# Kernel optimization log

Measured on AMD Instinct MI355X. Metric: run time of the kernel, lower is better.

The kernel has to match this reference:

```python
import jax, jax.numpy as jnp
import numpy as np

B, C, H, W, K = 2, 64, 192, 384, 8

def setup_inputs():
    key = jax.random.key(0)
    k1, k2, k3, k4, k5, k6 = jax.random.split(key, 6)
    feat = jax.random.normal(k1, (B, C, H, W), dtype=jnp.float32)
    mask_high = jax.random.randint(k2, (B, 1, H, W), 0, 2).astype(bool)
    Wo = jax.random.normal(k3, (2 * K, C), dtype=jnp.float32) * 0.1  # offset_conv 1x1 weight
    bo = jax.random.normal(k4, (2 * K,), dtype=jnp.float32) * 0.1
    Ww = jax.random.normal(k5, (K, C), dtype=jnp.float32) * 0.1     # weight_conv 1x1 weight
    bw = jax.random.normal(k6, (K,), dtype=jnp.float32) * 0.1
    return {"feat": feat, "mask_high": mask_high, "Wo": Wo, "bo": bo, "Ww": Ww, "bw": bw}

def _bilinear_sample(feat, px, py):
    # feat [B,C,H,W]; px,py [B,K,H,W] in pixel coords.
    # Matches F.grid_sample(mode='bilinear', padding_mode='zeros', align_corners=True)
    Bs, Cs, Hs, Ws = feat.shape
    Ks = px.shape[1]
    x0 = jnp.floor(px); y0 = jnp.floor(py)
    wx = px - x0; wy = py - y0
    x0i = x0.astype(jnp.int32); y0i = y0.astype(jnp.int32)
    feat_flat = feat.reshape(Bs, 1, Cs, Hs * Ws)
    def corner(xi, yi, w):
        valid = (xi >= 0) & (xi < Ws) & (yi >= 0) & (yi < Hs)
        idx = jnp.clip(yi, 0, Hs - 1) * Ws + jnp.clip(xi, 0, Ws - 1)
        g = jnp.take_along_axis(feat_flat, idx.reshape(Bs, Ks, 1, Hs * Ws), axis=-1)
        g = g.reshape(Bs, Ks, Cs, Hs, Ws)
        return g * (w * valid)[:, :, None]  # zero out-of-bounds corners
    return (corner(x0i, y0i, (1 - wx) * (1 - wy))
            + corner(x0i + 1, y0i, wx * (1 - wy))
            + corner(x0i, y0i + 1, (1 - wx) * wy)
            + corner(x0i + 1, y0i + 1, wx * wy))

def reference(feat, mask_high, Wo, bo, Ww, bw):
    Bs, Cs, Hs, Ws = feat.shape
    # 1x1 convs as channel contractions
    offsets = jnp.einsum('oc,bchw->bohw', Wo, feat) + bo[None, :, None, None]  # [B,2K,H,W]
    logits = jnp.einsum('kc,bchw->bkhw', Ww, feat) + bw[None, :, None, None]   # [B,K,H,W]
    weights = jax.nn.softmax(logits, axis=1)
    # base grid linspace(-1,1) with align_corners=True maps exactly to pixel coords;
    # dx/((W-1)/2) in normalized space == dx pixels, so sample point = (x+dx, y+dy)
    xs = jnp.arange(Ws, dtype=feat.dtype)
    ys = jnp.arange(Hs, dtype=feat.dtype)
    px = xs[None, None, None, :] + offsets[:, 0::2]  # [B,K,H,W]
    py = ys[None, None, :, None] + offsets[:, 1::2]
    sampled = _bilinear_sample(feat, px, py)          # [B,K,C,H,W]
    residual = jnp.einsum('bkchw,bkhw->bchw', sampled, weights)
    return feat + residual * mask_high.astype(feat.dtype)
```

## Files before the change

kernel.cpp:

```cpp
#include <hip/hip_runtime.h>
#include <hip/hip_fp16.h>

#define B_ 2
#define C_ 64
#define H_ 192
#define W_ 384
#define K_ 8
constexpr int HW_ = H_ * W_;
constexpr int CHW_ = C_ * HW_;
constexpr int NP_ = B_ * HW_;
constexpr int NBLK_ = NP_ / 64;
constexpr size_t WS_NEED_ = (size_t)NP_ * 64 * sizeof(unsigned short);

typedef _Float16 h8 __attribute__((ext_vector_type(8)));
typedef float f32x4 __attribute__((ext_vector_type(4)));

static __device__ __forceinline__ __half2 u2h(uint u) {
  union { uint u; __half2 h; } x; x.u = u; return x.h;
}
static __device__ __forceinline__ uint h2u(__half2 h) {
  union { uint u; __half2 h; } x; x.h = h; return x.u;
}

__global__ __launch_bounds__(256) void transposeh_kernel(
    const float* __restrict__ feat, unsigned short* __restrict__ ft) {
  __shared__ float lds[64 * 65];
  const int tid = threadIdx.x;
  const int lane = tid & 63;
  const int wv = tid >> 6;
  const int bid = blockIdx.x;
  const int sb = (bid & 7) * (NBLK_ / 8) + (bid >> 3);
  const int p0 = sb * 64;
  const int b = p0 / HW_;
  const int hw0 = p0 - b * HW_;
  const float* fb = feat + (size_t)b * CHW_;
#pragma unroll
  for (int cc = 0; cc < 16; ++cc) {
    const int c = wv * 16 + cc;
    lds[lane * 65 + c] = fb[(size_t)c * HW_ + hw0 + lane];
  }
  __syncthreads();
  uint* ft32 = (uint*)ft;
#pragma unroll
  for (int j = 0; j < 8; ++j) {
    const int idx = j * 256 + tid;
    const int row = idx >> 5;
    const int cp = idx & 31;
    const __half2 h = __floats2half2_rn(lds[row * 65 + 2 * cp],
                                        lds[row * 65 + 2 * cp + 1]);
    ft32[(size_t)(p0 + row) * 32 + cp] = h2u(h);
  }
}

__global__ __launch_bounds__(256) void mega_kernel(
    const int* __restrict__ mask,
    const float* __restrict__ Wo, const float* __restrict__ bo,
    const float* __restrict__ Ww, const float* __restrict__ bw,
    const unsigned short* __restrict__ ws, float* __restrict__ out) {
  __shared__ uint smem[6272];
  const unsigned short* sth = (const unsigned short*)smem;
  float* clds = (float*)(smem + 2304);
  uint4* reco = (uint4*)smem;
  uint4* recw = (uint4*)(smem + 2048);
  uint* resb = smem + 4096;
  int* actl = (int*)(smem + 6208);

  const int tid = threadIdx.x;
  const int lane = tid & 63;
  const int wv = tid >> 6;
  const int bid = blockIdx.x;
  const int sb = (bid & 7) * (NBLK_ / 8) + (bid >> 3);
  const int p0 = sb * 64;
  const int b = p0 / HW_;
  const int hw0 = p0 - b * HW_;
  const size_t bCHW = (size_t)b * CHW_;
  const int bHW = b * HW_;

  const uint4* ftq = (const uint4*)ws;
#pragma unroll
  for (int e = 0; e < 2; ++e) {
    const int j = tid * 2 + e;
    const int row = j >> 3;
    const int q = j & 7;
    const uint4 v = ftq[(size_t)p0 * 8 + j];
    *(uint4*)(smem + row * 36 + q * 4) = v;
  }
  const bool act = (mask[p0 + lane] != 0);
  const unsigned long long mball = __ballot(act);
  const int A = __popcll(mball);
#pragma unroll
  for (int j = 0; j < 9; ++j) {
    const int idx = j * 256 + tid;
    if (idx < 2112) resb[idx] = 0u;
  }
  __syncthreads();

  const int mrow = lane & 15;
  const int kq = lane >> 4;
  h8 afr[2][2];
#pragma unroll
  for (int mt = 0; mt < 2; ++mt) {
    const int row = mt * 16 + mrow;
    const float* wrow = (row < 16) ? (Wo + row * 64)
                                   : (Ww + (((row - 16) < 8 ? (row - 16) : 7) * 64));
    const float z = (row < 24) ? 1.f : 0.f;
#pragma unroll
    for (int k0 = 0; k0 < 2; ++k0) {
      const float4 a = *(const float4*)(wrow + k0 * 32 + kq * 8);
      const float4 bq = *(const float4*)(wrow + k0 * 32 + kq * 8 + 4);
      h8 h;
      h[0] = (_Float16)(a.x * z);  h[1] = (_Float16)(a.y * z);
      h[2] = (_Float16)(a.z * z);  h[3] = (_Float16)(a.w * z);
      h[4] = (_Float16)(bq.x * z); h[5] = (_Float16)(bq.y * z);
      h[6] = (_Float16)(bq.z * z); h[7] = (_Float16)(bq.w * z);
      afr[mt][k0] = h;
    }
  }
  const int px = wv * 16 + mrow;
  f32x4 ac0 = {0.f, 0.f, 0.f, 0.f};
  f32x4 ac1 = {0.f, 0.f, 0.f, 0.f};
#pragma unroll
  for (int k0 = 0; k0 < 2; ++k0) {
    const h8 bf = *(const h8*)(sth + px * 72 + k0 * 32 + kq * 8);
    ac0 = __builtin_amdgcn_mfma_f32_16x16x32_f16(afr[0][k0], bf, ac0, 0, 0, 0);
    ac1 = __builtin_amdgcn_mfma_f32_16x16x32_f16(afr[1][k0], bf, ac1, 0, 0, 0);
  }
#pragma unroll
  for (int r = 0; r < 4; ++r) clds[(kq * 4 + r) * 64 + px] = ac0[r];
  if (kq < 2) {
#pragma unroll
    for (int r = 0; r < 4; ++r) clds[(16 + kq * 4 + r) * 64 + px] = ac1[r];
  }
  __syncthreads();

  float acc[24];
#pragma unroll
  for (int j = 0; j < 24; ++j) acc[j] = clds[j * 64 + lane];
  __syncthreads();

#pragma unroll
  for (int j = 0; j < 16; ++j) acc[j] += bo[j];
#pragma unroll
  for (int j = 0; j < 8; ++j) acc[16 + j] += bw[j];
  float m = acc[16];
#pragma unroll
  for (int k = 1; k < K_; ++k) m = fmaxf(m, acc[16 + k]);
  float s = 0.f;
#pragma unroll
  for (int k = 0; k < K_; ++k) s += __expf(acc[16 + k] - m);
  const float inv = (act ? 1.f : 0.f) / s;

  const int hw = hw0 + lane;
  const int y = hw / W_;
  const int x = hw - y * W_;

#pragma unroll
  for (int t = 0; t < 2; ++t) {
    const int k = wv * 2 + t;
    const float wtk = __expf(acc[16 + k] - m) * inv;
    const float pxf = (float)x + acc[2 * k];
    const float pyf = (float)y + acc[2 * k + 1];
    const float x0f = floorf(pxf), y0f = floorf(pyf);
    const float wx = pxf - x0f, wy = pyf - y0f;
    const int x0 = (int)x0f, y0 = (int)y0f;
    const int x1 = x0 + 1, y1 = y0 + 1;
    const bool vx0 = ((unsigned)x0 < (unsigned)W_);
    const bool vx1 = ((unsigned)x1 < (unsigned)W_);
    const bool vy0 = ((unsigned)y0 < (unsigned)H_);
    const bool vy1 = ((unsigned)y1 < (unsigned)H_);
    const int cx0 = min(max(x0, 0), W_ - 1), cx1 = min(max(x1, 0), W_ - 1);
    const int cy0 = min(max(y0, 0), H_ - 1), cy1 = min(max(y1, 0), H_ - 1);
    const float w00 = wtk * (1.f - wx) * (1.f - wy) * ((vx0 && vy0) ? 1.f : 0.f);
    const float w01 = wtk * wx * (1.f - wy) * ((vx1 && vy0) ? 1.f : 0.f);
    const float w10 = wtk * (1.f - wx) * wy * ((vx0 && vy1) ? 1.f : 0.f);
    const float w11 = wtk * wx * wy * ((vx1 && vy1) ? 1.f : 0.f);
    uint4 o;
    o.x = act ? (uint)((bHW + cy0 * W_ + cx0) << 7) : 0u;
    o.y = act ? (uint)((bHW + cy0 * W_ + cx1) << 7) : 0u;
    o.z = act ? (uint)((bHW + cy1 * W_ + cx0) << 7) : 0u;
    o.w = act ? (uint)((bHW + cy1 * W_ + cx1) << 7) : 0u;
    uint4 wq;
    wq.x = h2u(__float2half2_rn(w00));
    wq.y = h2u(__float2half2_rn(w01));
    wq.z = h2u(__float2half2_rn(w10));
    wq.w = h2u(__float2half2_rn(w11));
    reco[k * 64 + lane] = o;
    recw[k * 64 + lane] = wq;
  }
  {
    const int aidx = __builtin_amdgcn_mbcnt_hi(
        (unsigned)(mball >> 32), __builtin_amdgcn_mbcnt_lo((unsigned)mball, 0));
    if (act) actl[aidx] = lane;
    if (A > 0) {
      const int first = __ffsll((unsigned long long)mball) - 1;
      if (lane >= A) actl[lane] = first;
    }
  }
  __syncthreads();

  const int pg = lane >> 3;
  const int cg = lane & 7;
  const int cgb = cg * 16;
  const char* ftb = (const char*)ws;
  const int tot = (A + 7) >> 3;

#define ACCH(V, WU)                                                        \
  do {                                                                     \
    const __half2 wh_ = u2h(WU);                                           \
    rr0 = __hfma2(wh_, u2h((V).x), rr0);                                   \
    rr1 = __hfma2(wh_, u2h((V).y), rr1);                                   \
    rr2 = __hfma2(wh_, u2h((V).z), rr2);                                   \
    rr3 = __hfma2(wh_, u2h((V).w), rr3);                                   \
  } while (0)

  for (int i = wv; i < tot; i += 4) {
    const int gi = i * 8 + pg;
    const int pxl = actl[gi];
    __half2 rr0 = __float2half2_rn(0.f), rr1 = rr0, rr2 = rr0, rr3 = rr0;
#pragma unroll
    for (int k2 = 0; k2 < 4; ++k2) {
      const int k0 = 2 * k2, k1 = 2 * k2 + 1;
      const uint4 o0 = reco[k0 * 64 + pxl];
      const uint4 w0 = recw[k0 * 64 + pxl];
      const uint4 o1 = reco[k1 * 64 + pxl];
      const uint4 w1 = recw[k1 * 64 + pxl];
      const uint4 v0 = *(const uint4*)(ftb + (o0.x + cgb));
      const uint4 v1 = *(const uint4*)(ftb + (o0.y + cgb));
      const uint4 v2 = *(const uint4*)(ftb + (o0.z + cgb));
      const uint4 v3 = *(const uint4*)(ftb + (o0.w + cgb));
      const uint4 v4 = *(const uint4*)(ftb + (o1.x + cgb));
      const uint4 v5 = *(const uint4*)(ftb + (o1.y + cgb));
      const uint4 v6 = *(const uint4*)(ftb + (o1.z + cgb));
      const uint4 v7 = *(const uint4*)(ftb + (o1.w + cgb));
      ACCH(v0, w0.x); ACCH(v1, w0.y); ACCH(v2, w0.z); ACCH(v3, w0.w);
      ACCH(v4, w1.x); ACCH(v5, w1.y); ACCH(v6, w1.z); ACCH(v7, w1.w);
    }
    if (gi < A) {
      const int base = pxl * 33 + cg * 4;
      resb[base + 0] = h2u(rr0);
      resb[base + 1] = h2u(rr1);
      resb[base + 2] = h2u(rr2);
      resb[base + 3] = h2u(rr3);
    }
  }
#undef ACCH
  __syncthreads();

  const uint* ft32 = (const uint*)ws;
  const size_t ftrow = (size_t)(p0 + lane) * 32;
#pragma unroll
  for (int cc = 0; cc < 8; ++cc) {
    const int cp = wv * 8 + cc;
    const float2 fv = __half22float2(u2h(ft32[ftrow + cp]));
    const float2 rv = __half22float2(u2h(resb[lane * 33 + cp]));
    const size_t off = bCHW + (size_t)(2 * cp) * HW_ + hw0 + lane;
    out[off] = fv.x + rv.x;
    out[off + HW_] = fv.y + rv.y;
  }
}

__global__ __launch_bounds__(256) void fused_kernel(
    const float* __restrict__ feat, const int* __restrict__ mask,
    const float* __restrict__ Wo, const float* __restrict__ bo,
    const float* __restrict__ Ww, const float* __restrict__ bw,
    float* __restrict__ out) {
  const int p = blockIdx.x * blockDim.x + threadIdx.x;
  const int b = p / HW_;
  const int hw = p - b * HW_;
  const int y = hw / W_;
  const int x = hw - y * W_;
  const float* fb = feat + b * CHW_;
  float acc[24];
#pragma unroll
  for (int i = 0; i < 16; ++i) acc[i] = bo[i];
#pragma unroll
  for (int i = 0; i < 8; ++i) acc[16 + i] = bw[i];
#pragma unroll
  for (int c = 0; c < C_; ++c) {
    const float v = fb[c * HW_ + hw];
#pragma unroll
    for (int i = 0; i < 16; ++i) acc[i] = fmaf(Wo[i * C_ + c], v, acc[i]);
#pragma unroll
    for (int i = 0; i < 8; ++i) acc[16 + i] = fmaf(Ww[i * C_ + c], v, acc[16 + i]);
  }
  float m = acc[16];
#pragma unroll
  for (int k = 1; k < K_; ++k) m = fmaxf(m, acc[16 + k]);
  float wt[K_];
  float s = 0.f;
#pragma unroll
  for (int k = 0; k < K_; ++k) { wt[k] = __expf(acc[16 + k] - m); s += wt[k]; }
  const float fm = (mask[p] != 0) ? 1.f : 0.f;
  const float inv = fm / s;
#pragma unroll
  for (int k = 0; k < K_; ++k) wt[k] *= inv;
  float res[C_];
#pragma unroll
  for (int c = 0; c < C_; ++c) res[c] = 0.f;
  if (fm != 0.f) {
#pragma unroll
    for (int k = 0; k < K_; ++k) {
      const float px = (float)x + acc[2 * k];
      const float py = (float)y + acc[2 * k + 1];
      const float x0f = floorf(px), y0f = floorf(py);
      const float wx = px - x0f, wy = py - y0f;
      const int x0 = (int)x0f, y0 = (int)y0f;
      const int x1 = x0 + 1, y1 = y0 + 1;
      const bool vx0 = ((unsigned)x0 < (unsigned)W_);
      const bool vx1 = ((unsigned)x1 < (unsigned)W_);
      const bool vy0 = ((unsigned)y0 < (unsigned)H_);
      const bool vy1 = ((unsigned)y1 < (unsigned)H_);
      const int cx0 = min(max(x0, 0), W_ - 1), cx1 = min(max(x1, 0), W_ - 1);
      const int cy0 = min(max(y0, 0), H_ - 1), cy1 = min(max(y1, 0), H_ - 1);
      const float wk = wt[k];
      const float w00 = wk * (1.f - wx) * (1.f - wy) * ((vx0 && vy0) ? 1.f : 0.f);
      const float w01 = wk * wx * (1.f - wy) * ((vx1 && vy0) ? 1.f : 0.f);
      const float w10 = wk * (1.f - wx) * wy * ((vx0 && vy1) ? 1.f : 0.f);
      const float w11 = wk * wx * wy * ((vx1 && vy1) ? 1.f : 0.f);
      const int i00 = cy0 * W_ + cx0, i01 = cy0 * W_ + cx1;
      const int i10 = cy1 * W_ + cx0, i11 = cy1 * W_ + cx1;
#pragma unroll
      for (int c = 0; c < C_; ++c) {
        const float* fc = fb + c * HW_;
        res[c] += w00 * fc[i00] + w01 * fc[i01] + w10 * fc[i10] + w11 * fc[i11];
      }
    }
  }
#pragma unroll
  for (int c = 0; c < C_; ++c)
    out[b * CHW_ + c * HW_ + hw] = fb[c * HW_ + hw] + res[c];
}

extern "C" void kernel_launch(void* const* d_in, const int* in_sizes, int n_in,
                              void* d_out, int out_size, void* d_ws, size_t ws_size,
                              hipStream_t stream) {
  const float* feat = (const float*)d_in[0];
  const int* mask = (const int*)d_in[1];
  const float* Wo = (const float*)d_in[2];
  const float* bo = (const float*)d_in[3];
  const float* Ww = (const float*)d_in[4];
  const float* bw = (const float*)d_in[5];
  float* out = (float*)d_out;

  if (ws_size >= WS_NEED_) {
    unsigned short* ft = (unsigned short*)d_ws;
    hipLaunchKernelGGL(transposeh_kernel, dim3(NBLK_), dim3(256), 0, stream,
                       feat, ft);
    hipLaunchKernelGGL(mega_kernel, dim3(NBLK_), dim3(256), 0, stream,
                       mask, Wo, bo, Ww, bw, ft, out);
  } else {
    hipLaunchKernelGGL(fused_kernel, dim3(NP_ / 256), dim3(256), 0, stream,
                       feat, mask, Wo, bo, Ww, bw, out);
  }
}
```

Before: 42.17 us.

## Read MFMA operands from global, pack bilinear weights, trim LDS and a barrier

Drops the LDS staging of the 64-pixel fp16 feature tile and loads the MFMA B fragments directly from global memory, which removes one __syncthreads and shrinks shared memory. The active-pixel list is built earlier, the per-corner weights are packed as half pairs (uint2 instead of uint4) and broadcast with half2 shuffles, and the act-based zeroing of corner offsets is removed. Lower LDS use may allow more blocks per CU, at the cost of uncoalesced direct global reads for the MFMA operands and extra broadcast instructions in the gather loop.

```diff
diff --git a/kernel.cpp b/kernel.cpp
--- a/kernel.cpp
+++ b/kernel.cpp
@@ -57,13 +57,12 @@
     const float* __restrict__ Wo, const float* __restrict__ bo,
     const float* __restrict__ Ww, const float* __restrict__ bw,
     const unsigned short* __restrict__ ws, float* __restrict__ out) {
-  __shared__ uint smem[6272];
-  const unsigned short* sth = (const unsigned short*)smem;
-  float* clds = (float*)(smem + 2304);
+  __shared__ uint smem[5248];
+  float* clds = (float*)smem;
   uint4* reco = (uint4*)smem;
-  uint4* recw = (uint4*)(smem + 2048);
-  uint* resb = smem + 4096;
-  int* actl = (int*)(smem + 6208);
+  uint2* rwt = (uint2*)(smem + 2048);
+  uint* resb = smem + 3072;
+  int* actl = (int*)(smem + 5184);
 
   const int tid = threadIdx.x;
   const int lane = tid & 63;
@@ -76,24 +75,23 @@
   const size_t bCHW = (size_t)b * CHW_;
   const int bHW = b * HW_;
 
-  const uint4* ftq = (const uint4*)ws;
-#pragma unroll
-  for (int e = 0; e < 2; ++e) {
-    const int j = tid * 2 + e;
-    const int row = j >> 3;
-    const int q = j & 7;
-    const uint4 v = ftq[(size_t)p0 * 8 + j];
-    *(uint4*)(smem + row * 36 + q * 4) = v;
-  }
   const bool act = (mask[p0 + lane] != 0);
   const unsigned long long mball = __ballot(act);
   const int A = __popcll(mball);
+  {
+    const int aidx = __builtin_amdgcn_mbcnt_hi(
+        (unsigned)(mball >> 32), __builtin_amdgcn_mbcnt_lo((unsigned)mball, 0));
+    if (act) actl[aidx] = lane;
+    if (A > 0) {
+      const int first = __ffsll((unsigned long long)mball) - 1;
+      if (lane >= A) actl[lane] = first;
+    }
+  }
 #pragma unroll
   for (int j = 0; j < 9; ++j) {
     const int idx = j * 256 + tid;
     if (idx < 2112) resb[idx] = 0u;
   }
-  __syncthreads();
 
   const int mrow = lane & 15;
   const int kq = lane >> 4;
@@ -117,11 +115,12 @@
     }
   }
   const int px = wv * 16 + mrow;
+  const _Float16* ftp = (const _Float16*)ws;
   f32x4 ac0 = {0.f, 0.f, 0.f, 0.f};
   f32x4 ac1 = {0.f, 0.f, 0.f, 0.f};
 #pragma unroll
   for (int k0 = 0; k0 < 2; ++k0) {
-    const h8 bf = *(const h8*)(sth + px * 72 + k0 * 32 + kq * 8);
+    const h8 bf = *(const h8*)(ftp + (size_t)(p0 + px) * 64 + k0 * 32 + kq * 8);
     ac0 = __builtin_amdgcn_mfma_f32_16x16x32_f16(afr[0][k0], bf, ac0, 0, 0, 0);
     ac1 = __builtin_amdgcn_mfma_f32_16x16x32_f16(afr[1][k0], bf, ac1, 0, 0, 0);
   }
@@ -175,26 +174,15 @@
     const float w10 = wtk * (1.f - wx) * wy * ((vx0 && vy1) ? 1.f : 0.f);
     const float w11 = wtk * wx * wy * ((vx1 && vy1) ? 1.f : 0.f);
     uint4 o;
-    o.x = act ? (uint)((bHW + cy0 * W_ + cx0) << 7) : 0u;
-    o.y = act ? (uint)((bHW + cy0 * W_ + cx1) << 7) : 0u;
-    o.z = act ? (uint)((bHW + cy1 * W_ + cx0) << 7) : 0u;
-    o.w = act ? (uint)((bHW + cy1 * W_ + cx1) << 7) : 0u;
-    uint4 wq;
-    wq.x = h2u(__float2half2_rn(w00));
-    wq.y = h2u(__float2half2_rn(w01));
-    wq.z = h2u(__float2half2_rn(w10));
-    wq.w = h2u(__float2half2_rn(w11));
+    o.x = (uint)((bHW + cy0 * W_ + cx0) << 7);
+    o.y = (uint)((bHW + cy0 * W_ + cx1) << 7);
+    o.z = (uint)((bHW + cy1 * W_ + cx0) << 7);
+    o.w = (uint)((bHW + cy1 * W_ + cx1) << 7);
+    uint2 wq;
+    wq.x = h2u(__floats2half2_rn(w00, w01));
+    wq.y = h2u(__floats2half2_rn(w10, w11));
     reco[k * 64 + lane] = o;
-    recw[k * 64 + lane] = wq;
-  }
-  {
-    const int aidx = __builtin_amdgcn_mbcnt_hi(
-        (unsigned)(mball >> 32), __builtin_amdgcn_mbcnt_lo((unsigned)mball, 0));
-    if (act) actl[aidx] = lane;
-    if (A > 0) {
-      const int first = __ffsll((unsigned long long)mball) - 1;
-      if (lane >= A) actl[lane] = first;
-    }
+    rwt[k * 64 + lane] = wq;
   }
   __syncthreads();
 
@@ -204,13 +192,12 @@
   const char* ftb = (const char*)ws;
   const int tot = (A + 7) >> 3;
 
-#define ACCH(V, WU)                                                        \
+#define ACCH(V, WH)                                                        \
   do {                                                                     \
-    const __half2 wh_ = u2h(WU);                                           \
-    rr0 = __hfma2(wh_, u2h((V).x), rr0);                                   \
-    rr1 = __hfma2(wh_, u2h((V).y), rr1);                                   \
-    rr2 = __hfma2(wh_, u2h((V).z), rr2);                                   \
-    rr3 = __hfma2(wh_, u2h((V).w), rr3);                                   \
+    rr0 = __hfma2(WH, u2h((V).x), rr0);                                    \
+    rr1 = __hfma2(WH, u2h((V).y), rr1);                                    \
+    rr2 = __hfma2(WH, u2h((V).z), rr2);                                    \
+    rr3 = __hfma2(WH, u2h((V).w), rr3);                                    \
   } while (0)
 
   for (int i = wv; i < tot; i += 4) {
@@ -221,9 +208,9 @@
     for (int k2 = 0; k2 < 4; ++k2) {
       const int k0 = 2 * k2, k1 = 2 * k2 + 1;
       const uint4 o0 = reco[k0 * 64 + pxl];
-      const uint4 w0 = recw[k0 * 64 + pxl];
+      const uint2 wp0 = rwt[k0 * 64 + pxl];
       const uint4 o1 = reco[k1 * 64 + pxl];
-      const uint4 w1 = recw[k1 * 64 + pxl];
+      const uint2 wp1 = rwt[k1 * 64 + pxl];
       const uint4 v0 = *(const uint4*)(ftb + (o0.x + cgb));
       const uint4 v1 = *(const uint4*)(ftb + (o0.y + cgb));
       const uint4 v2 = *(const uint4*)(ftb + (o0.z + cgb));
@@ -232,8 +219,16 @@
       const uint4 v5 = *(const uint4*)(ftb + (o1.y + cgb));
       const uint4 v6 = *(const uint4*)(ftb + (o1.z + cgb));
       const uint4 v7 = *(const uint4*)(ftb + (o1.w + cgb));
-      ACCH(v0, w0.x); ACCH(v1, w0.y); ACCH(v2, w0.z); ACCH(v3, w0.w);
-      ACCH(v4, w1.x); ACCH(v5, w1.y); ACCH(v6, w1.z); ACCH(v7, w1.w);
+      const __half2 a0 = u2h(wp0.x), b0 = u2h(wp0.y);
+      const __half2 a1 = u2h(wp1.x), b1 = u2h(wp1.y);
+      ACCH(v0, __half2half2(__low2half(a0)));
+      ACCH(v1, __half2half2(__high2half(a0)));
+      ACCH(v2, __half2half2(__low2half(b0)));
+      ACCH(v3, __half2half2(__high2half(b0)));
+      ACCH(v4, __half2half2(__low2half(a1)));
+      ACCH(v5, __half2half2(__high2half(a1)));
+      ACCH(v6, __half2half2(__low2half(b1)));
+      ACCH(v7, __half2half2(__high2half(b1)));
     }
     if (gi < A) {
       const int base = pxl * 33 + cg * 4;
```

Result: no change. 42.80 us (+1.5%).
